# Kernel optimization log

Measured on AMD Instinct MI355X. Metric: run time of the kernel, lower is better.

## Reference

```python
import jax, jax.numpy as jnp
import numpy as np

DIM = 256
HEADS = 8
HEAD_DIM = DIM // HEADS
WS = 7            # window size
SHIFT = 3         # shift size
H = 56
W = 56
B = 32
WA = WS * WS      # window area = 49
NWH, NWW = H // WS, W // WS
NW = NWH * NWW    # windows per image


def _make_attn_mask():
    # replicate the torch mask construction for the shifted windows
    img = np.zeros((H, W), dtype=np.float32)
    cnt = 0
    for hs in (slice(0, -WS), slice(-WS, -SHIFT), slice(-SHIFT, None)):
        for ws_ in (slice(0, -WS), slice(-WS, -SHIFT), slice(-SHIFT, None)):
            img[hs, ws_] = cnt
            cnt += 1
    mw = img.reshape(NWH, WS, NWW, WS).transpose(0, 2, 1, 3).reshape(-1, WA)  # (nW, 49)
    diff = mw[:, None, :] - mw[:, :, None]                                    # (nW, 49, 49)
    return np.where(diff != 0, -100.0, 0.0).astype(np.float32)


def _make_rel_index():
    coords = np.stack(np.meshgrid(np.arange(WS), np.arange(WS), indexing='ij')).reshape(2, -1)
    rel = coords[:, :, None] - coords[:, None, :]        # (2, 49, 49)
    rel = rel.transpose(1, 2, 0) + (WS - 1)              # shift to >= 0
    rel[..., 0] *= 2 * WS - 1
    return rel.sum(-1).astype(np.int32)                  # (49, 49) in [0, 169)


def setup_inputs() -> dict:
    key = jax.random.key(0)
    ks = jax.random.split(key, 12)
    s = 0.02
    inp = {
        'x': jax.random.normal(ks[0], (B, H, W, DIM), dtype=jnp.float32),
        'ln1_w': jnp.ones((DIM,), jnp.float32), 'ln1_b': jnp.zeros((DIM,), jnp.float32),
        'qkv_w': s * jax.random.normal(ks[1], (3 * DIM, DIM), jnp.float32),
        'qkv_b': jnp.zeros((3 * DIM,), jnp.float32),
        'rpb_table': s * jax.random.normal(ks[2], ((2 * WS - 1) ** 2, HEADS), jnp.float32),
        'proj_w': s * jax.random.normal(ks[3], (DIM, DIM), jnp.float32),
        'proj_b': jnp.zeros((DIM,), jnp.float32),
        'ln2_w': jnp.ones((DIM,), jnp.float32), 'ln2_b': jnp.zeros((DIM,), jnp.float32),
        'fc1_w': s * jax.random.normal(ks[4], (4 * DIM, DIM), jnp.float32),
        'fc1_b': jnp.zeros((4 * DIM,), jnp.float32),
        'ln3_w': jnp.ones((4 * DIM,), jnp.float32), 'ln3_b': jnp.zeros((4 * DIM,), jnp.float32),
        'fc2_w': s * jax.random.normal(ks[5], (DIM, 4 * DIM), jnp.float32),
        'fc2_b': jnp.zeros((DIM,), jnp.float32),
        'attn_mask': jnp.asarray(_make_attn_mask()),     # (nW, 49, 49)
        'rel_index': jnp.asarray(_make_rel_index()),     # (49, 49) int32
    }
    return inp


def _ln(x, w, b, eps=1e-5):
    m = jnp.mean(x, axis=-1, keepdims=True)
    v = jnp.mean((x - m) ** 2, axis=-1, keepdims=True)
    return (x - m) * jax.lax.rsqrt(v + eps) * w + b


def reference(x, ln1_w, ln1_b, qkv_w, qkv_b, rpb_table, proj_w, proj_b,
              ln2_w, ln2_b, fc1_w, fc1_b, ln3_w, ln3_b, fc2_w, fc2_b,
              attn_mask, rel_index):
    Bn, Hn, Wn, C = x.shape
    # ---- attention branch ----
    y = _ln(x, ln1_w, ln1_b)
    sh = jnp.roll(y, (-SHIFT, -SHIFT), axis=(1, 2))
    # window partition: (B, H, W, C) -> (B*nW, 49, C)
    win = sh.reshape(Bn, NWH, WS, NWW, WS, C).transpose(0, 1, 3, 2, 4, 5).reshape(Bn * NW, WA, C)
    qkv = win @ qkv_w.T + qkv_b                              # (Bw, 49, 3C)
    qkv = qkv.reshape(Bn * NW, WA, 3, HEADS, HEAD_DIM).transpose(2, 0, 3, 1, 4)
    q, k, v = qkv[0], qkv[1], qkv[2]                         # (Bw, h, 49, d)
    scale = HEAD_DIM ** -0.5
    attn = jnp.einsum('bhqd,bhkd->bhqk', q * scale, k)       # (Bw, h, 49, 49)
    bias = rpb_table[rel_index]                              # (49, 49, h)
    attn = attn + jnp.transpose(bias, (2, 0, 1))[None]
    attn = attn.reshape(Bn, NW, HEADS, WA, WA) + attn_mask[None, :, None]
    attn = jax.nn.softmax(attn, axis=-1).reshape(Bn * NW, HEADS, WA, WA)
    out = jnp.einsum('bhqk,bhkd->bhqd', attn, v)             # (Bw, h, 49, d)
    out = out.transpose(0, 2, 1, 3).reshape(Bn * NW, WA, C)
    out = out @ proj_w.T + proj_b
    # window reverse + un-shift
    out = out.reshape(Bn, NWH, NWW, WS, WS, C).transpose(0, 1, 3, 2, 4, 5).reshape(Bn, Hn, Wn, C)
    out = jnp.roll(out, (SHIFT, SHIFT), axis=(1, 2))
    x = x + out
    # ---- MLP branch (note: extra LayerNorm inside MLP per source) ----
    z = _ln(x, ln2_w, ln2_b)
    h = jax.nn.gelu(z @ fc1_w.T + fc1_b, approximate=False)
    h = _ln(h, ln3_w, ln3_b)
    x = x + (h @ fc2_w.T + fc2_b)
    return x
```

## Files before the change

kernel.cpp:

```cpp
#include <hip/hip_runtime.h>
#include <hip/hip_bf16.h>
#include <math.h>

typedef __attribute__((ext_vector_type(8))) short bf16x8;
typedef __attribute__((ext_vector_type(4))) float f32x4;
typedef __attribute__((ext_vector_type(4))) float f4;
typedef __attribute__((ext_vector_type(8))) unsigned short us8;
typedef __attribute__((ext_vector_type(4))) unsigned short us4;
typedef unsigned short u16;
typedef unsigned int u32;

#define HEADS 8
#define SHIFT_ 3
#define HIMG 56
#define WIMG 56
#define WA 49
#define NTOK 100352
#define NPAIR 16384

static __device__ __forceinline__ float bf2f(u16 v){ return __uint_as_float(((u32)v)<<16); }
static __device__ __forceinline__ u16 f2bf(float f){
  u32 u = __float_as_uint(f);
  return (u16)((u + 0x7fffu + ((u>>16)&1u)) >> 16);
}
static __device__ __forceinline__ float wsum(float v){
  #pragma unroll
  for (int off=32; off>0; off>>=1) v += __shfl_xor(v, off, 64);
  return v;
}
static __device__ __forceinline__ void glds16(const u16* g, u16* l){
  __builtin_amdgcn_global_load_lds(
      (const __attribute__((address_space(1))) unsigned int*)g,
      (__attribute__((address_space(3))) unsigned int*)l, 16, 0, 0);
}
static __device__ __forceinline__ int tok2pix(int row){
  int bw = row / 49, t = row - bw*49;
  int b  = bw >> 6,  w = bw & 63;
  int wh = w >> 3,   ww = w & 7;
  int th = t / 7,    tw = t - th*7;
  int r = wh*7 + th + SHIFT_; if (r >= HIMG) r -= HIMG;
  int c = ww*7 + tw + SHIFT_; if (c >= WIMG) c -= WIMG;
  return (b*HIMG + r)*WIMG + c;
}
static __device__ __forceinline__ float gelu_f(float x){
  float z  = 0.70710678118654752f * x;
  float az = fabsf(z);
  float t  = __builtin_amdgcn_rcpf(1.0f + 0.3275911f*az);
  float p  = t*(0.254829592f + t*(-0.284496736f + t*(1.421413741f + t*(-1.453152027f + t*1.061405429f))));
  float er = 1.0f - p*__expf(-z*z);
  er = (x < 0.0f) ? -er : er;
  return 0.5f*x*(1.0f + er);
}

template<int C, int ISBF>
__global__ void ln_stats_kernel(const void* __restrict__ srcv, float* __restrict__ stats){
  int wave = threadIdx.x >> 6, lane = threadIdx.x & 63;
  int tok = blockIdx.x*4 + wave;
  float s=0.f, s2=0.f;
  if (ISBF == 0){
    const float* p = (const float*)srcv + (size_t)tok*C;
    #pragma unroll
    for (int i=0;i<C/256;i++){
      f4 v = *(const f4*)(p + lane*4*(C/256) + i*4);
      #pragma unroll
      for (int e=0;e<4;e++){ float f=v[e]; s+=f; s2+=f*f; }
    }
  } else {
    const u16* p = (const u16*)srcv + (size_t)tok*C;
    #pragma unroll
    for (int i=0;i<C/512;i++){
      us8 v = *(const us8*)(p + lane*8*(C/512) + i*8);
      #pragma unroll
      for (int e=0;e<8;e++){ float f=bf2f(v[e]); s+=f; s2+=f*f; }
    }
  }
  s = wsum(s); s2 = wsum(s2);
  if (lane==0){
    float mean = s/(float)C;
    float var  = s2/(float)C - mean*mean;
    stats[2*tok]   = mean;
    stats[2*tok+1] = rsqrtf(var + 1e-5f);
  }
}

__global__ void ln_apply_kernel(const float* __restrict__ src, u16* __restrict__ dst){
  int wave = threadIdx.x >> 6, lane = threadIdx.x & 63;
  int tok = blockIdx.x*4 + wave;
  const float* p = src + (size_t)tok*256;
  f4 a = *(const f4*)(p + lane*4);
  float s = a[0]+a[1]+a[2]+a[3];
  float s2 = a[0]*a[0]+a[1]*a[1]+a[2]*a[2]+a[3]*a[3];
  s = wsum(s); s2 = wsum(s2);
  float mean = s*(1.f/256.f);
  float var  = s2*(1.f/256.f) - mean*mean;
  float rstd = rsqrtf(var + 1e-5f);
  us4 o;
  #pragma unroll
  for (int e=0;e<4;e++) o[e] = f2bf((a[e]-mean)*rstd);
  *(us4*)(dst + (size_t)tok*256 + lane*4) = o;
}

__global__ void prep_weights(
    const float* __restrict__ qkv_w, const float* __restrict__ qkv_b,
    const float* __restrict__ ln1w,  const float* __restrict__ ln1b,
    const float* __restrict__ fc1_w, const float* __restrict__ fc1_b,
    const float* __restrict__ ln2w,  const float* __restrict__ ln2b,
    const float* __restrict__ fc2_w, const float* __restrict__ fc2_b,
    const float* __restrict__ ln3w,  const float* __restrict__ ln3b,
    const float* __restrict__ proj_w, const float* __restrict__ proj_b,
    u16* __restrict__ wq, float* __restrict__ bq,
    u16* __restrict__ w1, float* __restrict__ b1,
    u16* __restrict__ w2, float* __restrict__ b2,
    u16* __restrict__ wp, float* __restrict__ bp)
{
  int wave = threadIdx.x>>6, lane = threadIdx.x&63;
  int n = blockIdx.x*4 + wave;
  const float *W,*lw,*lb,*bs; u16* WO; float* BO; int K, row, noln;
  if (n < 768)      { W=qkv_w; lw=ln1w; lb=ln1b; bs=qkv_b; WO=wq; BO=bq; K=256;  row=n;      noln=0; }
  else if (n < 1792){ W=fc1_w; lw=ln2w; lb=ln2b; bs=fc1_b; WO=w1; BO=b1; K=256;  row=n-768;  noln=0; }
  else if (n < 2048){ W=fc2_w; lw=ln3w; lb=ln3b; bs=fc2_b; WO=w2; BO=b2; K=1024; row=n-1792; noln=0; }
  else              { W=proj_w; lw=nullptr; lb=nullptr; bs=proj_b; WO=wp; BO=bp; K=256; row=n-2048; noln=1; }
  float dot = 0.f;
  for (int k=lane; k<K; k+=64){
    float wv = W[(size_t)row*K + k];
    if (noln){
      WO[(size_t)row*K + k] = f2bf(wv);
    } else {
      dot += wv * lb[k];
      WO[(size_t)row*K + k] = f2bf(wv * lw[k]);
    }
  }
  dot = wsum(dot);
  if (lane==0) BO[row] = bs[row] + dot;
}

template<int SMODE, int EPI>
__global__ __launch_bounds__(256)
void gemm5(const void* __restrict__ Av, const u16* __restrict__ Bt,
           const float* __restrict__ stats, const float* __restrict__ biasf,
           const float* __restrict__ resid, void* __restrict__ outv,
           int K, int NT, int CHUNK)
{
  constexpr int BM=128, BN=128, BK=64;
  __shared__ u16 smem[16384];
  u16* As = smem;
  u16* Bs = smem + 8192;
  int b = blockIdx.x;
  int linear = (b & 7)*CHUNK + (b >> 3);
  int mt = linear / NT, nt = linear - mt*NT;
  int m0 = mt*BM, n0 = nt*BN;
  int tid  = threadIdx.x;
  int lane = tid & 63, wave = tid >> 6;
  int wr = wave >> 1, wc = wave & 1;
  int lc16 = lane & 15, g = lane >> 4;
  int nsteps = K >> 6;

  const u16* asrc[4];
  const u16* bsrc[4];
  #pragma unroll
  for (int i=0;i<4;i++){
    int c = tid + i*256;
    int row = c >> 3, ch = (c & 7) ^ (row & 7);
    if (SMODE <= 1){
      int grow = (SMODE==0) ? tok2pix(m0+row) : (m0+row);
      asrc[i] = (const u16*)Av + (size_t)grow*K + ch*8;
    }
    bsrc[i] = Bt + (size_t)(n0+row)*K + ch*8;
  }
  float smean[4], srstd[4];
  if (SMODE >= 2){
    #pragma unroll
    for (int i=0;i<4;i++){
      int grow = m0 + ((tid + i*256) >> 3);
      smean[i] = stats[2*grow]; srstd[i] = stats[2*grow+1];
    }
  }

  f32x4 acc[4][4];
  #pragma unroll
  for (int i=0;i<4;i++)
    #pragma unroll
    for (int j=0;j<4;j++){ acc[i][j][0]=0.f; acc[i][j][1]=0.f; acc[i][j][2]=0.f; acc[i][j][3]=0.f; }

  us8 rcur[4]; f4 rcurf[4][2];
  if (SMODE >= 2){
    #pragma unroll
    for (int i=0;i<4;i++){
      int c = tid + i*256; int row = c>>3, ch = c&7;
      if (SMODE==2) rcur[i] = *(const us8*)((const u16*)Av + (size_t)(m0+row)*K + ch*8);
      else {
        const float* ap = (const float*)Av + (size_t)(m0+row)*K + ch*8;
        rcurf[i][0] = *(const f4*)ap; rcurf[i][1] = *(const f4*)(ap+4);
      }
    }
  }

  for (int t=0; t<nsteps; ++t){
    int kt = t << 6;
    if (SMODE <= 1){
      #pragma unroll
      for (int i=0;i<4;i++) glds16(asrc[i]+kt, As + i*2048 + wave*512);
    } else {
      #pragma unroll
      for (int i=0;i<4;i++){
        int c = tid + i*256; int row = c>>3, ch = c&7;
        us8 o;
        #pragma unroll
        for (int e=0;e<8;e++){
          float fv = (SMODE==2) ? bf2f(rcur[i][e]) : rcurf[i][e>>2][e&3];
          o[e] = f2bf((fv - smean[i])*srstd[i]);
        }
        u32 byte = (u32)(row*128 + ch*16) ^ ((u32)(row&7)<<4);
        *(us8*)(As + (byte>>1)) = o;
      }
    }
    #pragma unroll
    for (int i=0;i<4;i++) glds16(bsrc[i]+kt, Bs + i*2048 + wave*512);
    __syncthreads();
    if (SMODE >= 2 && t+1 < nsteps){
      int kt1 = kt + 64;
      us8 rnext[4]; f4 rnextf[4][2];
      #pragma unroll
      for (int i=0;i<4;i++){
        int c = tid + i*256; int row = c>>3, ch = c&7;
        if (SMODE==2) rnext[i] = *(const us8*)((const u16*)Av + (size_t)(m0+row)*K + kt1 + ch*8);
        else {
          const float* ap = (const float*)Av + (size_t)(m0+row)*K + kt1 + ch*8;
          rnextf[i][0] = *(const f4*)ap; rnextf[i][1] = *(const f4*)(ap+4);
        }
      }
      #pragma unroll
      for (int kk=0; kk<2; kk++){
        bf16x8 af[4], bfr[4];
        #pragma unroll
        for (int mi=0;mi<4;mi++){
          int r = wr*64 + mi*16 + lc16;
          u32 byte = (u32)(r*128 + kk*64 + g*16) ^ ((u32)(r&7)<<4);
          af[mi] = *(const bf16x8*)(As + (byte>>1));
        }
        #pragma unroll
        for (int ni=0;ni<4;ni++){
          int r = wc*64 + ni*16 + lc16;
          u32 byte = (u32)(r*128 + kk*64 + g*16) ^ ((u32)(r&7)<<4);
          bfr[ni] = *(const bf16x8*)(Bs + (byte>>1));
        }
        #pragma unroll
        for (int mi=0;mi<4;mi++)
          #pragma unroll
          for (int ni=0;ni<4;ni++)
            acc[mi][ni] = __builtin_amdgcn_mfma_f32_16x16x32_bf16(af[mi], bfr[ni], acc[mi][ni], 0, 0, 0);
      }
      #pragma unroll
      for (int i=0;i<4;i++){
        if (SMODE==2) rcur[i] = rnext[i];
        else { rcurf[i][0] = rnextf[i][0]; rcurf[i][1] = rnextf[i][1]; }
      }
    } else {
      #pragma unroll
      for (int kk=0; kk<2; kk++){
        bf16x8 af[4], bfr[4];
        #pragma unroll
        for (int mi=0;mi<4;mi++){
          int r = wr*64 + mi*16 + lc16;
          u32 byte = (u32)(r*128 + kk*64 + g*16) ^ ((u32)(r&7)<<4);
          af[mi] = *(const bf16x8*)(As + (byte>>1));
        }
        #pragma unroll
        for (int ni=0;ni<4;ni++){
          int r = wc*64 + ni*16 + lc16;
          u32 byte = (u32)(r*128 + kk*64 + g*16) ^ ((u32)(r&7)<<4);
          bfr[ni] = *(const bf16x8*)(Bs + (byte>>1));
        }
        #pragma unroll
        for (int mi=0;mi<4;mi++)
          #pragma unroll
          for (int ni=0;ni<4;ni++)
            acc[mi][ni] = __builtin_amdgcn_mfma_f32_16x16x32_bf16(af[mi], bfr[ni], acc[mi][ni], 0, 0, 0);
      }
    }
    __syncthreads();
  }

  int lr = lane >> 4;
  if (EPI==0 || EPI==2){
    u16* Cs = smem;
    #pragma unroll
    for (int mi=0;mi<4;mi++){
      #pragma unroll
      for (int ni=0;ni<4;ni++){
        int cl = wc*64 + ni*16 + lc16;
        float bv = biasf[n0 + cl];
        #pragma unroll
        for (int j=0;j<4;j++){
          int rl = wr*64 + mi*16 + lr*4 + j;
          float v = acc[mi][ni][j] + bv;
          if (EPI==2) v = gelu_f(v);
          u32 byte = (u32)(rl*256 + cl*2) ^ ((u32)(rl&7)<<4);
          Cs[byte>>1] = f2bf(v);
        }
      }
    }
    __syncthreads();
    #pragma unroll
    for (int i=0;i<8;i++){
      int c = tid + i*256;
      int rl = c>>4, c0 = (c&15)*8;
      u32 byte = (u32)(rl*256 + c0*2) ^ ((u32)(rl&7)<<4);
      us8 v = *(const us8*)(Cs + (byte>>1));
      int row = m0 + rl, col = n0 + c0;
      if (EPI==0){
        int which = col>>8, hh = (col>>5)&7, d0 = col&31;
        int bwi = row/49, t = row - bwi*49;
        *(us8*)((u16*)outv + ((size_t)which*NPAIR + bwi*8 + hh)*(WA*32) + t*32 + d0) = v;
      } else {
        *(us8*)((u16*)outv + (size_t)row*1024 + col) = v;
      }
    }
  } else {
    float* Cs = (float*)smem;
    #pragma unroll
    for (int hp=0; hp<2; hp++){
      if (hp) __syncthreads();
      if (wc == hp){
        #pragma unroll
        for (int mi=0;mi<4;mi++){
          #pragma unroll
          for (int ni=0;ni<4;ni++){
            int cl = ni*16 + lc16;
            float bv = biasf[n0 + hp*64 + cl];
            #pragma unroll
            for (int j=0;j<4;j++){
              int rl = wr*64 + mi*16 + lr*4 + j;
              u32 byte = (u32)(rl*256 + cl*4) ^ ((u32)(rl&7)<<4);
              *(float*)((char*)Cs + byte) = acc[mi][ni][j] + bv;
            }
          }
        }
      }
      __syncthreads();
      #pragma unroll
      for (int i=0;i<8;i++){
        int c = tid + i*256;
        int row = c>>4, ch = c&15;
        u32 byte = (u32)(row*256 + ch*16) ^ ((u32)(row&7)<<4);
        f4 v = *(const f4*)((const char*)Cs + byte);
        int grow = m0 + row, col = n0 + hp*64 + ch*4;
        size_t addr;
        if (EPI==1) addr = (size_t)tok2pix(grow)*256 + col;
        else        addr = (size_t)grow*256 + col;
        f4 rr = *(const f4*)(resid + addr);
        v += rr;
        *(f4*)((float*)outv + addr) = v;
      }
    }
  }
}

__global__ void attn_mfma_kernel(
    const u16* __restrict__ qkv,
    const float* __restrict__ rpb,
    const int* __restrict__ rel,
    const float* __restrict__ mask,
    u16* __restrict__ outb)
{
  __shared__ u16 Kls[4][64*32];
  __shared__ u16 Vt [4][32*64];
  __shared__ u16 Pls[4][64*64];
  int wave = threadIdx.x>>6, lane = threadIdx.x&63;
  int pair = blockIdx.x*4 + wave;
  int bw = pair>>3, h = pair&7, w = bw&63;
  int lc = lane&15, g = lane>>4;
  const u16* qg = qkv + (size_t)pair*(WA*32);
  const u16* kg = qg + (size_t)NPAIR*(WA*32);
  const u16* vg = qg + (size_t)2*NPAIR*(WA*32);
  u16* Kp = &Kls[wave][0];
  u16* Vp = &Vt[wave][0];
  u16* Pp = &Pls[wave][0];

  #pragma unroll
  for (int i=0;i<4;i++){
    int idx = i*64 + lane;
    int r = idx>>2, seg = idx&3;
    us8 kv, vv;
    if (r < WA){
      kv = *(const us8*)(kg + r*32 + seg*8);
      vv = *(const us8*)(vg + r*32 + seg*8);
    } else {
      #pragma unroll
      for (int e=0;e<8;e++){ kv[e]=0; vv[e]=0; }
    }
    *(us8*)(Kp + r*32 + seg*8) = kv;
    #pragma unroll
    for (int e=0;e<8;e++){
      int d = seg*8 + e;
      u32 byte = ((u32)(d*128 + r*2)) ^ ((u32)(d&7)<<4);
      Vp[byte>>1] = vv[e];
    }
  }

  bf16x8 qa[4];
  #pragma unroll
  for (int mi=0;mi<4;mi++){
    int r = mi*16 + lc;
    if (r < WA) qa[mi] = *(const bf16x8*)(qg + r*32 + g*8);
    else { bf16x8 z;
           #pragma unroll
           for (int e=0;e<8;e++) z[e]=0; qa[mi]=z; }
  }

  f32x4 acc[4][4];
  #pragma unroll
  for (int i=0;i<4;i++)
    #pragma unroll
    for (int j=0;j<4;j++){ acc[i][j][0]=0.f; acc[i][j][1]=0.f; acc[i][j][2]=0.f; acc[i][j][3]=0.f; }
  __syncthreads();
  #pragma unroll
  for (int ni=0;ni<4;ni++){
    bf16x8 kb = *(const bf16x8*)(Kp + (ni*16+lc)*32 + g*8);
    #pragma unroll
    for (int mi=0;mi<4;mi++)
      acc[mi][ni] = __builtin_amdgcn_mfma_f32_16x16x32_bf16(qa[mi], kb, acc[mi][ni], 0, 0, 0);
  }

  const float scale = 0.17677669529663689f;
  float rinv[4][4];
  #pragma unroll
  for (int mi=0;mi<4;mi++){
    #pragma unroll
    for (int jr=0;jr<4;jr++){
      int i = mi*16 + g*4 + jr;
      float sv[4];
      #pragma unroll
      for (int ni=0;ni<4;ni++){
        int j = ni*16 + lc;
        float s;
        if (i < WA && j < WA){
          s = acc[mi][ni][jr]*scale + rpb[rel[i*WA+j]*8 + h] + mask[((size_t)w*WA + i)*WA + j];
        } else s = -1e9f;
        sv[ni] = s;
      }
      float mx = fmaxf(fmaxf(sv[0],sv[1]), fmaxf(sv[2],sv[3]));
      #pragma unroll
      for (int off=1; off<16; off<<=1) mx = fmaxf(mx, __shfl_xor(mx, off, 64));
      float sum = 0.f;
      #pragma unroll
      for (int ni=0;ni<4;ni++){ sv[ni] = __expf(sv[ni]-mx); sum += sv[ni]; }
      #pragma unroll
      for (int off=1; off<16; off<<=1) sum += __shfl_xor(sum, off, 64);
      rinv[mi][jr] = __builtin_amdgcn_rcpf(sum);
      #pragma unroll
      for (int ni=0;ni<4;ni++){
        int j = ni*16 + lc;
        u32 byte = ((u32)(i*128 + j*2)) ^ ((u32)(i&7)<<4);
        Pp[byte>>1] = f2bf(sv[ni]);
      }
    }
  }

  bf16x8 vb[2][2];
  #pragma unroll
  for (int kk=0;kk<2;kk++)
    #pragma unroll
    for (int ni=0;ni<2;ni++){
      int d = ni*16 + lc;
      u32 byte = ((u32)(d*128 + kk*64 + g*16)) ^ ((u32)(d&7)<<4);
      vb[kk][ni] = *(const bf16x8*)(Vp + (byte>>1));
    }
  f32x4 aco[4][2];
  #pragma unroll
  for (int i=0;i<4;i++)
    #pragma unroll
    for (int j=0;j<2;j++){ aco[i][j][0]=0.f; aco[i][j][1]=0.f; aco[i][j][2]=0.f; aco[i][j][3]=0.f; }
  #pragma unroll
  for (int mi=0;mi<4;mi++){
    int r = mi*16 + lc;
    #pragma unroll
    for (int kk=0;kk<2;kk++){
      u32 byte = ((u32)(r*128 + kk*64 + g*16)) ^ ((u32)(r&7)<<4);
      bf16x8 pa = *(const bf16x8*)(Pp + (byte>>1));
      #pragma unroll
      for (int ni=0;ni<2;ni++)
        aco[mi][ni] = __builtin_amdgcn_mfma_f32_16x16x32_bf16(pa, vb[kk][ni], aco[mi][ni], 0, 0, 0);
    }
  }

  u16* Op = Kp;
  #pragma unroll
  for (int mi=0;mi<4;mi++){
    #pragma unroll
    for (int jr=0;jr<4;jr++){
      int i = mi*16 + g*4 + jr;
      if (i < WA){
        float rv = rinv[mi][jr];
        #pragma unroll
        for (int ni=0;ni<2;ni++)
          Op[i*32 + ni*16 + lc] = f2bf(aco[mi][ni][jr]*rv);
      }
    }
  }
  __syncthreads();
  size_t obase = (size_t)(bw*WA)*256 + h*32;
  #pragma unroll
  for (int i=0;i<4;i++){
    int c = i*64 + lane;
    if (c < WA*4){
      int t = c>>2, seg = c&3;
      *(us8*)(outb + obase + (size_t)t*256 + seg*8) = *(const us8*)(Op + t*32 + seg*8);
    }
  }
}

extern "C" void kernel_launch(void* const* d_in, const int* in_sizes, int n_in,
                              void* d_out, int out_size, void* d_ws, size_t ws_size,
                              hipStream_t stream) {
  const float* x      = (const float*)d_in[0];
  const float* ln1w   = (const float*)d_in[1];
  const float* ln1b   = (const float*)d_in[2];
  const float* qkv_w  = (const float*)d_in[3];
  const float* qkv_b  = (const float*)d_in[4];
  const float* rpb    = (const float*)d_in[5];
  const float* proj_w = (const float*)d_in[6];
  const float* proj_b = (const float*)d_in[7];
  const float* ln2w   = (const float*)d_in[8];
  const float* ln2b   = (const float*)d_in[9];
  const float* fc1_w  = (const float*)d_in[10];
  const float* fc1_b  = (const float*)d_in[11];
  const float* ln3w   = (const float*)d_in[12];
  const float* ln3b   = (const float*)d_in[13];
  const float* fc2_w  = (const float*)d_in[14];
  const float* fc2_b  = (const float*)d_in[15];
  const float* amask  = (const float*)d_in[16];
  const int*   rel    = (const int*)d_in[17];
  float* out = (float*)d_out;

  char* ws = (char*)d_ws;
  float* statsC = (float*)(ws);
  float* statsB = (float*)(ws +  802816);
  float* bq     = (float*)(ws + 1605632);
  float* b1     = (float*)(ws + 1608704);
  float* b2     = (float*)(ws + 1612800);
  float* bp     = (float*)(ws + 1613824);
  u16*   wq     = (u16*)  (ws + 1614848);
  u16*   w1     = (u16*)  (ws + 2008064);
  u16*   w2     = (u16*)  (ws + 2532352);
  u16*   wp     = (u16*)  (ws + 3056640);
  const size_t P0 = 3187712;
  u16*   qkvbuf = (u16*)(ws + P0);
  u16*   attno  = (u16*)(ws + P0 + 154140672);
  u16*   xb     = (u16*)(ws + P0 + 154140672);
  u16*   hbuf   = (u16*)(ws + P0);
  u16*   x1b    = (u16*)(ws + P0 + 205520896);
  const int bigws = (ws_size >= (size_t)(P0 + 205520896ull + 51380224ull));

  prep_weights<<<576,256,0,stream>>>(qkv_w,qkv_b,ln1w,ln1b, fc1_w,fc1_b,ln2w,ln2b,
                                     fc2_w,fc2_b,ln3w,ln3b, proj_w,proj_b,
                                     wq,bq, w1,b1, w2,b2, wp,bp);
  ln_apply_kernel<<<NTOK/4,256,0,stream>>>(x, xb);
  gemm5<0,0><<<784*6,256,0,stream>>>(xb, wq, nullptr, bq, nullptr, qkvbuf, 256, 6, 588);
  attn_mfma_kernel<<<NPAIR/4,256,0,stream>>>(qkvbuf, rpb, rel, amask, attno);
  gemm5<1,1><<<784*2,256,0,stream>>>(attno, wp, nullptr, bp, x, out, 256, 2, 196);
  if (bigws){
    ln_apply_kernel<<<NTOK/4,256,0,stream>>>(out, x1b);
    gemm5<1,2><<<784*8,256,0,stream>>>(x1b, w1, nullptr, b1, nullptr, hbuf, 256, 8, 784);
  } else {
    ln_stats_kernel<256,0><<<NTOK/4,256,0,stream>>>(out, statsB);
    gemm5<3,2><<<784*8,256,0,stream>>>(out, w1, statsB, b1, nullptr, hbuf, 256, 8, 784);
  }
  ln_stats_kernel<1024,1><<<NTOK/4,256,0,stream>>>(hbuf, statsC);
  gemm5<2,3><<<784*2,256,0,stream>>>(hbuf, w2, statsC, b2, out, out, 1024, 2, 196);
}
```

Measured before the change: 646.1 us.

## Fold LN3 normalization into fc2 epilogue via weight column sums; tanh GELU

The fc2 GEMM now reads the raw bf16 hidden activations straight into LDS through the async load path. The LayerNorm is applied algebraically in the epilogue as acc*rstd + bias - mean*rstd*colsum(W), with the column sums precomputed in prep_weights. This removes the per-element normalize and bf16 repack in the A-tile load loop. GELU switches from the erf polynomial to the tanh approximation, which is cheaper but less exact and may cancel more precision when mean and rstd are large.

```diff
diff --git a/kernel.cpp b/kernel.cpp
--- a/kernel.cpp
+++ b/kernel.cpp
@@ -43,13 +43,11 @@
   return (b*HIMG + r)*WIMG + c;
 }
 static __device__ __forceinline__ float gelu_f(float x){
-  float z  = 0.70710678118654752f * x;
-  float az = fabsf(z);
-  float t  = __builtin_amdgcn_rcpf(1.0f + 0.3275911f*az);
-  float p  = t*(0.254829592f + t*(-0.284496736f + t*(1.421413741f + t*(-1.453152027f + t*1.061405429f))));
-  float er = 1.0f - p*__expf(-z*z);
-  er = (x < 0.0f) ? -er : er;
-  return 0.5f*x*(1.0f + er);
+  float x2 = x*x;
+  float u  = x*(0.7978845608028654f + 0.0356774081363001f*x2);
+  float e  = __expf(u+u);
+  float th = 1.0f - 2.0f*__builtin_amdgcn_rcpf(1.0f+e);
+  return 0.5f*x*(1.0f+th);
 }
 
 template<int C, int ISBF>
@@ -111,35 +109,39 @@
     u16* __restrict__ wq, float* __restrict__ bq,
     u16* __restrict__ w1, float* __restrict__ b1,
     u16* __restrict__ w2, float* __restrict__ b2,
-    u16* __restrict__ wp, float* __restrict__ bp)
+    u16* __restrict__ wp, float* __restrict__ bp,
+    float* __restrict__ cs2)
 {
   int wave = threadIdx.x>>6, lane = threadIdx.x&63;
   int n = blockIdx.x*4 + wave;
-  const float *W,*lw,*lb,*bs; u16* WO; float* BO; int K, row, noln;
-  if (n < 768)      { W=qkv_w; lw=ln1w; lb=ln1b; bs=qkv_b; WO=wq; BO=bq; K=256;  row=n;      noln=0; }
-  else if (n < 1792){ W=fc1_w; lw=ln2w; lb=ln2b; bs=fc1_b; WO=w1; BO=b1; K=256;  row=n-768;  noln=0; }
-  else if (n < 2048){ W=fc2_w; lw=ln3w; lb=ln3b; bs=fc2_b; WO=w2; BO=b2; K=1024; row=n-1792; noln=0; }
-  else              { W=proj_w; lw=nullptr; lb=nullptr; bs=proj_b; WO=wp; BO=bp; K=256; row=n-2048; noln=1; }
-  float dot = 0.f;
+  const float *W,*lw,*lb,*bs; u16* WO; float* BO; int K, row, noln, docs;
+  if (n < 768)      { W=qkv_w; lw=ln1w; lb=ln1b; bs=qkv_b; WO=wq; BO=bq; K=256;  row=n;      noln=0; docs=0; }
+  else if (n < 1792){ W=fc1_w; lw=ln2w; lb=ln2b; bs=fc1_b; WO=w1; BO=b1; K=256;  row=n-768;  noln=0; docs=0; }
+  else if (n < 2048){ W=fc2_w; lw=ln3w; lb=ln3b; bs=fc2_b; WO=w2; BO=b2; K=1024; row=n-1792; noln=0; docs=1; }
+  else              { W=proj_w; lw=nullptr; lb=nullptr; bs=proj_b; WO=wp; BO=bp; K=256; row=n-2048; noln=1; docs=0; }
+  float dot = 0.f, cs = 0.f;
   for (int k=lane; k<K; k+=64){
     float wv = W[(size_t)row*K + k];
     if (noln){
       WO[(size_t)row*K + k] = f2bf(wv);
     } else {
       dot += wv * lb[k];
-      WO[(size_t)row*K + k] = f2bf(wv * lw[k]);
+      u16 q = f2bf(wv * lw[k]);
+      WO[(size_t)row*K + k] = q;
+      cs += bf2f(q);
     }
   }
   dot = wsum(dot);
+  if (docs){ cs = wsum(cs); if (lane==0) cs2[row] = cs; }
   if (lane==0) BO[row] = bs[row] + dot;
 }
 
 template<int SMODE, int EPI>
 __global__ __launch_bounds__(256)
-void gemm5(const void* __restrict__ Av, const u16* __restrict__ Bt,
+void gemm6(const void* __restrict__ Av, const u16* __restrict__ Bt,
            const float* __restrict__ stats, const float* __restrict__ biasf,
-           const float* __restrict__ resid, void* __restrict__ outv,
-           int K, int NT, int CHUNK)
+           const float* __restrict__ resid, const float* __restrict__ colsum,
+           void* __restrict__ outv, int K, int NT, int CHUNK)
 {
   constexpr int BM=128, BN=128, BK=64;
   __shared__ u16 smem[16384];
@@ -168,7 +170,7 @@
     bsrc[i] = Bt + (size_t)(n0+row)*K + ch*8;
   }
   float smean[4], srstd[4];
-  if (SMODE >= 2){
+  if (SMODE == 3){
     #pragma unroll
     for (int i=0;i<4;i++){
       int grow = m0 + ((tid + i*256) >> 3);
@@ -182,16 +184,13 @@
     #pragma unroll
     for (int j=0;j<4;j++){ acc[i][j][0]=0.f; acc[i][j][1]=0.f; acc[i][j][2]=0.f; acc[i][j][3]=0.f; }
 
-  us8 rcur[4]; f4 rcurf[4][2];
-  if (SMODE >= 2){
+  f4 rcurf[4][2];
+  if (SMODE == 3){
     #pragma unroll
     for (int i=0;i<4;i++){
       int c = tid + i*256; int row = c>>3, ch = c&7;
-      if (SMODE==2) rcur[i] = *(const us8*)((const u16*)Av + (size_t)(m0+row)*K + ch*8);
-      else {
-        const float* ap = (const float*)Av + (size_t)(m0+row)*K + ch*8;
-        rcurf[i][0] = *(const f4*)ap; rcurf[i][1] = *(const f4*)(ap+4);
-      }
+      const float* ap = (const float*)Av + (size_t)(m0+row)*K + ch*8;
+      rcurf[i][0] = *(const f4*)ap; rcurf[i][1] = *(const f4*)(ap+4);
     }
   }
 
@@ -207,7 +206,7 @@
         us8 o;
         #pragma unroll
         for (int e=0;e<8;e++){
-          float fv = (SMODE==2) ? bf2f(rcur[i][e]) : rcurf[i][e>>2][e&3];
+          float fv = rcurf[i][e>>2][e&3];
           o[e] = f2bf((fv - smean[i])*srstd[i]);
         }
         u32 byte = (u32)(row*128 + ch*16) ^ ((u32)(row&7)<<4);
@@ -217,17 +216,14 @@
     #pragma unroll
     for (int i=0;i<4;i++) glds16(bsrc[i]+kt, Bs + i*2048 + wave*512);
     __syncthreads();
-    if (SMODE >= 2 && t+1 < nsteps){
+    if (SMODE == 3 && t+1 < nsteps){
       int kt1 = kt + 64;
-      us8 rnext[4]; f4 rnextf[4][2];
+      f4 rnextf[4][2];
       #pragma unroll
       for (int i=0;i<4;i++){
         int c = tid + i*256; int row = c>>3, ch = c&7;
-        if (SMODE==2) rnext[i] = *(const us8*)((const u16*)Av + (size_t)(m0+row)*K + kt1 + ch*8);
-        else {
-          const float* ap = (const float*)Av + (size_t)(m0+row)*K + kt1 + ch*8;
-          rnextf[i][0] = *(const f4*)ap; rnextf[i][1] = *(const f4*)(ap+4);
-        }
+        const float* ap = (const float*)Av + (size_t)(m0+row)*K + kt1 + ch*8;
+        rnextf[i][0] = *(const f4*)ap; rnextf[i][1] = *(const f4*)(ap+4);
       }
       #pragma unroll
       for (int kk=0; kk<2; kk++){
@@ -251,10 +247,7 @@
             acc[mi][ni] = __builtin_amdgcn_mfma_f32_16x16x32_bf16(af[mi], bfr[ni], acc[mi][ni], 0, 0, 0);
       }
       #pragma unroll
-      for (int i=0;i<4;i++){
-        if (SMODE==2) rcur[i] = rnext[i];
-        else { rcurf[i][0] = rnextf[i][0]; rcurf[i][1] = rnextf[i][1]; }
-      }
+      for (int i=0;i<4;i++){ rcurf[i][0] = rnextf[i][0]; rcurf[i][1] = rnextf[i][1]; }
     } else {
       #pragma unroll
       for (int kk=0; kk<2; kk++){
@@ -322,17 +315,32 @@
     for (int hp=0; hp<2; hp++){
       if (hp) __syncthreads();
       if (wc == hp){
+        float bv4[4], cs4[4];
+        #pragma unroll
+        for (int ni=0;ni<4;ni++){
+          int col = n0 + hp*64 + ni*16 + lc16;
+          bv4[ni] = biasf[col];
+          if (EPI==4) cs4[ni] = colsum[col];
+        }
         #pragma unroll
         for (int mi=0;mi<4;mi++){
           #pragma unroll
-          for (int ni=0;ni<4;ni++){
-            int cl = ni*16 + lc16;
-            float bv = biasf[n0 + hp*64 + cl];
+          for (int j=0;j<4;j++){
+            int rl = wr*64 + mi*16 + lr*4 + j;
+            float rs = 1.f, mmrs = 0.f;
+            if (EPI==4){
+              int grow = m0 + rl;
+              rs = stats[2*grow+1];
+              mmrs = stats[2*grow]*rs;
+            }
             #pragma unroll
-            for (int j=0;j<4;j++){
-              int rl = wr*64 + mi*16 + lr*4 + j;
+            for (int ni=0;ni<4;ni++){
+              int cl = ni*16 + lc16;
+              float v;
+              if (EPI==4) v = acc[mi][ni][j]*rs + bv4[ni] - mmrs*cs4[ni];
+              else        v = acc[mi][ni][j] + bv4[ni];
               u32 byte = (u32)(rl*256 + cl*4) ^ ((u32)(rl&7)<<4);
-              *(float*)((char*)Cs + byte) = acc[mi][ni][j] + bv;
+              *(float*)((char*)Cs + byte) = v;
             }
           }
         }
@@ -540,11 +548,12 @@
   float* b1     = (float*)(ws + 1608704);
   float* b2     = (float*)(ws + 1612800);
   float* bp     = (float*)(ws + 1613824);
-  u16*   wq     = (u16*)  (ws + 1614848);
-  u16*   w1     = (u16*)  (ws + 2008064);
-  u16*   w2     = (u16*)  (ws + 2532352);
-  u16*   wp     = (u16*)  (ws + 3056640);
-  const size_t P0 = 3187712;
+  float* cs2    = (float*)(ws + 1614848);
+  u16*   wq     = (u16*)  (ws + 1615872);
+  u16*   w1     = (u16*)  (ws + 2009088);
+  u16*   w2     = (u16*)  (ws + 2533376);
+  u16*   wp     = (u16*)  (ws + 3057664);
+  const size_t P0 = 3188736;
   u16*   qkvbuf = (u16*)(ws + P0);
   u16*   attno  = (u16*)(ws + P0 + 154140672);
   u16*   xb     = (u16*)(ws + P0 + 154140672);
@@ -554,18 +563,18 @@
 
   prep_weights<<<576,256,0,stream>>>(qkv_w,qkv_b,ln1w,ln1b, fc1_w,fc1_b,ln2w,ln2b,
                                      fc2_w,fc2_b,ln3w,ln3b, proj_w,proj_b,
-                                     wq,bq, w1,b1, w2,b2, wp,bp);
+                                     wq,bq, w1,b1, w2,b2, wp,bp, cs2);
   ln_apply_kernel<<<NTOK/4,256,0,stream>>>(x, xb);
-  gemm5<0,0><<<784*6,256,0,stream>>>(xb, wq, nullptr, bq, nullptr, qkvbuf, 256, 6, 588);
+  gemm6<0,0><<<784*6,256,0,stream>>>(xb, wq, nullptr, bq, nullptr, nullptr, qkvbuf, 256, 6, 588);
   attn_mfma_kernel<<<NPAIR/4,256,0,stream>>>(qkvbuf, rpb, rel, amask, attno);
-  gemm5<1,1><<<784*2,256,0,stream>>>(attno, wp, nullptr, bp, x, out, 256, 2, 196);
+  gemm6<1,1><<<784*2,256,0,stream>>>(attno, wp, nullptr, bp, x, nullptr, out, 256, 2, 196);
   if (bigws){
     ln_apply_kernel<<<NTOK/4,256,0,stream>>>(out, x1b);
-    gemm5<1,2><<<784*8,256,0,stream>>>(x1b, w1, nullptr, b1, nullptr, hbuf, 256, 8, 784);
+    gemm6<1,2><<<784*8,256,0,stream>>>(x1b, w1, nullptr, b1, nullptr, nullptr, hbuf, 256, 8, 784);
   } else {
     ln_stats_kernel<256,0><<<NTOK/4,256,0,stream>>>(out, statsB);
-    gemm5<3,2><<<784*8,256,0,stream>>>(out, w1, statsB, b1, nullptr, hbuf, 256, 8, 784);
+    gemm6<3,2><<<784*8,256,0,stream>>>(out, w1, statsB, b1, nullptr, nullptr, hbuf, 256, 8, 784);
   }
   ln_stats_kernel<1024,1><<<NTOK/4,256,0,stream>>>(hbuf, statsC);
-  gemm5<2,3><<<784*2,256,0,stream>>>(hbuf, w2, statsC, b2, out, out, 1024, 2, 196);
-}
+  gemm6<1,4><<<784*2,256,0,stream>>>(hbuf, w2, statsC, b2, out, cs2, out, 1024, 2, 196);
+}
```

Result: faster. 626.7 us (-3.0%).
